# Kernel optimization log

Measured on AMD Instinct MI355X. Metric: run time of the kernel, lower is better.

Reference implementation:

```python
import jax, jax.numpy as jnp
import numpy as np

MAX_SEQ_LEN = 512          # offset added to pairwise diffs
NUM_HEADS = 12             # per-table embedding dim and fused output dim
TABLE_SIZE = 2 * MAX_SEQ_LEN + 1  # 1025
BATCH, SEQ = 4, 512


def setup_inputs() -> dict:
    key = jax.random.key(0)
    ks = jax.random.split(key, 8)
    pos_s = jnp.sort(jax.random.randint(ks[0], (BATCH, SEQ), 0, MAX_SEQ_LEN, dtype=jnp.int32), axis=-1)
    pos_e = jnp.sort(jax.random.randint(ks[1], (BATCH, SEQ), 0, MAX_SEQ_LEN, dtype=jnp.int32), axis=-1)
    pe_ss = jax.random.normal(ks[2], (TABLE_SIZE, NUM_HEADS), dtype=jnp.float32)
    pe_se = jax.random.normal(ks[3], (TABLE_SIZE, NUM_HEADS), dtype=jnp.float32)
    pe_es = jax.random.normal(ks[4], (TABLE_SIZE, NUM_HEADS), dtype=jnp.float32)
    pe_ee = jax.random.normal(ks[5], (TABLE_SIZE, NUM_HEADS), dtype=jnp.float32)
    W = jax.random.normal(ks[6], (4 * NUM_HEADS, NUM_HEADS), dtype=jnp.float32) / np.sqrt(4 * NUM_HEADS)
    b = jax.random.normal(ks[7], (NUM_HEADS,), dtype=jnp.float32) * 0.01
    return {"pos_s": pos_s, "pos_e": pos_e, "pe_ss": pe_ss, "pe_se": pe_se,
            "pe_es": pe_es, "pe_ee": pe_ee, "W": W, "b": b}


def reference(pos_s, pos_e, pe_ss, pe_se, pe_es, pe_ee, W, b):
    # pairwise distance indices, each [B, S, S], values in [0, 2*MAX_SEQ_LEN]
    idx_ss = pos_s[:, :, None] - pos_s[:, None, :] + MAX_SEQ_LEN
    idx_se = pos_s[:, :, None] - pos_e[:, None, :] + MAX_SEQ_LEN
    idx_es = pos_e[:, :, None] - pos_s[:, None, :] + MAX_SEQ_LEN
    idx_ee = pos_e[:, :, None] - pos_e[:, None, :] + MAX_SEQ_LEN
    # four gathers -> [B, S, S, H] each; concat on feature axis -> [B, S, S, 4H]
    pe4 = jnp.concatenate([pe_ss[idx_ss], pe_se[idx_se], pe_es[idx_es], pe_ee[idx_ee]], axis=-1)
    # Linear(4H -> H) + ReLU, then permute to [B, H, S, S]
    fused = jax.nn.relu(jnp.einsum('bijf,fh->bijh', pe4, W) + b)
    return jnp.transpose(fused, (0, 3, 1, 2))
```

## Files before the change

kernel.cpp:

```cpp
#include <hip/hip_runtime.h>

#define MAX_SEQ_LEN 512
#define NUM_HEADS 12
#define TABLE_SIZE 1025
#define BATCH 4
#define SEQ 512

__global__ void proj_tables_kernel(const float* __restrict__ pe_ss,
                                   const float* __restrict__ pe_se,
                                   const float* __restrict__ pe_es,
                                   const float* __restrict__ pe_ee,
                                   const float* __restrict__ W,
                                   const float* __restrict__ bias,
                                   float* __restrict__ proj) {
    int tid = blockIdx.x * blockDim.x + threadIdx.x;
    if (tid >= 4 * TABLE_SIZE) return;
    int t   = tid / TABLE_SIZE;
    int idx = tid - t * TABLE_SIZE;

    const float* pe = (t == 0 ? pe_ss : t == 1 ? pe_se : t == 2 ? pe_es : pe_ee)
                      + idx * NUM_HEADS;
    float pev[NUM_HEADS];
#pragma unroll
    for (int f = 0; f < NUM_HEADS; ++f) pev[f] = pe[f];

    float* out = proj + (size_t)tid * NUM_HEADS;
#pragma unroll
    for (int h = 0; h < NUM_HEADS; ++h) {
        float acc = (t == 0) ? bias[h] : 0.0f;
#pragma unroll
        for (int f = 0; f < NUM_HEADS; ++f)
            acc += pev[f] * W[(t * NUM_HEADS + f) * NUM_HEADS + h];
        out[h] = acc;
    }
}

__global__ __launch_bounds__(128)
void fuse_kernel(const int* __restrict__ pos_s,
                 const int* __restrict__ pos_e,
                 const float* __restrict__ proj,
                 float* __restrict__ out) {
    const int bi = blockIdx.x;
    const int b  = bi >> 9;
    const int i  = bi & (SEQ - 1);

    const int ps_i = pos_s[b * SEQ + i];
    const int pe_i = pos_e[b * SEQ + i];

    const int j0 = threadIdx.x * 4;
    const int4 js4 = *reinterpret_cast<const int4*>(pos_s + b * SEQ + j0);
    const int4 je4 = *reinterpret_cast<const int4*>(pos_e + b * SEQ + j0);
    const int jsa[4] = {js4.x, js4.y, js4.z, js4.w};
    const int jea[4] = {je4.x, je4.y, je4.z, je4.w};

    const float* __restrict__ pss = proj;
    const float* __restrict__ pse = proj + 1 * TABLE_SIZE * NUM_HEADS;
    const float* __restrict__ pes = proj + 2 * TABLE_SIZE * NUM_HEADS;
    const float* __restrict__ pee = proj + 3 * TABLE_SIZE * NUM_HEADS;

    float acc[4][NUM_HEADS];

#pragma unroll
    for (int k = 0; k < 4; ++k) {
        const int iss = ps_i - jsa[k] + MAX_SEQ_LEN;
        const int ise = ps_i - jea[k] + MAX_SEQ_LEN;
        const int ies = pe_i - jsa[k] + MAX_SEQ_LEN;
        const int iee = pe_i - jea[k] + MAX_SEQ_LEN;

        const float4* r0 = reinterpret_cast<const float4*>(pss + iss * NUM_HEADS);
        const float4* r1 = reinterpret_cast<const float4*>(pse + ise * NUM_HEADS);
        const float4* r2 = reinterpret_cast<const float4*>(pes + ies * NUM_HEADS);
        const float4* r3 = reinterpret_cast<const float4*>(pee + iee * NUM_HEADS);

        float4 a0 = r0[0], a1 = r0[1], a2 = r0[2];
        float4 b0 = r1[0], b1 = r1[1], b2 = r1[2];
        float4 c0 = r2[0], c1 = r2[1], c2 = r2[2];
        float4 d0 = r3[0], d1 = r3[1], d2 = r3[2];

        acc[k][0]  = a0.x + b0.x + c0.x + d0.x;
        acc[k][1]  = a0.y + b0.y + c0.y + d0.y;
        acc[k][2]  = a0.z + b0.z + c0.z + d0.z;
        acc[k][3]  = a0.w + b0.w + c0.w + d0.w;
        acc[k][4]  = a1.x + b1.x + c1.x + d1.x;
        acc[k][5]  = a1.y + b1.y + c1.y + d1.y;
        acc[k][6]  = a1.z + b1.z + c1.z + d1.z;
        acc[k][7]  = a1.w + b1.w + c1.w + d1.w;
        acc[k][8]  = a2.x + b2.x + c2.x + d2.x;
        acc[k][9]  = a2.y + b2.y + c2.y + d2.y;
        acc[k][10] = a2.z + b2.z + c2.z + d2.z;
        acc[k][11] = a2.w + b2.w + c2.w + d2.w;
    }

    float* obase = out + (((size_t)b * NUM_HEADS) * SEQ + i) * SEQ + j0;
#pragma unroll
    for (int h = 0; h < NUM_HEADS; ++h) {
        float4 v;
        v.x = fmaxf(acc[0][h], 0.0f);
        v.y = fmaxf(acc[1][h], 0.0f);
        v.z = fmaxf(acc[2][h], 0.0f);
        v.w = fmaxf(acc[3][h], 0.0f);
        *reinterpret_cast<float4*>(obase + (size_t)h * SEQ * SEQ) = v;
    }
}

extern "C" void kernel_launch(void* const* d_in, const int* in_sizes, int n_in,
                              void* d_out, int out_size, void* d_ws, size_t ws_size,
                              hipStream_t stream) {
    const int*   pos_s = (const int*)d_in[0];
    const int*   pos_e = (const int*)d_in[1];
    const float* pe_ss = (const float*)d_in[2];
    const float* pe_se = (const float*)d_in[3];
    const float* pe_es = (const float*)d_in[4];
    const float* pe_ee = (const float*)d_in[5];
    const float* W     = (const float*)d_in[6];
    const float* bias  = (const float*)d_in[7];
    float* out  = (float*)d_out;
    float* proj = (float*)d_ws;

    {
        int total = 4 * TABLE_SIZE;
        int block = 256;
        int grid  = (total + block - 1) / block;
        proj_tables_kernel<<<grid, block, 0, stream>>>(pe_ss, pe_se, pe_es, pe_ee,
                                                       W, bias, proj);
    }

    {
        dim3 grid(BATCH * SEQ);
        dim3 block(128);
        fuse_kernel<<<grid, block, 0, stream>>>(pos_s, pos_e, proj, out);
    }
}
```

Measured before the change: 114.1 us.

## Stage per-row summed projection windows in LDS before pairwise gather

Each block, which handles one (b,i) row, now loads the 512-entry window of projected tables that its fixed pos_s[i] and pos_e[i] can reach. It pre-adds ss+es and se+ee into two LDS arrays, so each output element needs two LDS row reads instead of four scattered global reads. Blocks grow to 256 threads with two j per thread and float2 stores. The exchange is a per-block staging pass of about 48KB of global reads plus a barrier, and narrower output stores.

```diff
diff --git a/kernel.cpp b/kernel.cpp
--- a/kernel.cpp
+++ b/kernel.cpp
@@ -5,6 +5,9 @@
 #define TABLE_SIZE 1025
 #define BATCH 4
 #define SEQ 512
+#define ROWF 12
+#define WIN 512
+#define F4_PER_WIN (WIN * ROWF / 4)
 
 __global__ void proj_tables_kernel(const float* __restrict__ pe_ss,
                                    const float* __restrict__ pe_se,
@@ -24,82 +27,82 @@
 #pragma unroll
     for (int f = 0; f < NUM_HEADS; ++f) pev[f] = pe[f];
 
-    float* out = proj + (size_t)tid * NUM_HEADS;
+    float* outp = proj + (size_t)tid * NUM_HEADS;
 #pragma unroll
     for (int h = 0; h < NUM_HEADS; ++h) {
         float acc = (t == 0) ? bias[h] : 0.0f;
 #pragma unroll
         for (int f = 0; f < NUM_HEADS; ++f)
             acc += pev[f] * W[(t * NUM_HEADS + f) * NUM_HEADS + h];
-        out[h] = acc;
+        outp[h] = acc;
     }
 }
 
-__global__ __launch_bounds__(128)
+__global__ __launch_bounds__(256)
 void fuse_kernel(const int* __restrict__ pos_s,
                  const int* __restrict__ pos_e,
                  const float* __restrict__ proj,
                  float* __restrict__ out) {
+    __shared__ float4 ldsA[F4_PER_WIN];
+    __shared__ float4 ldsB[F4_PER_WIN];
+
     const int bi = blockIdx.x;
     const int b  = bi >> 9;
     const int i  = bi & (SEQ - 1);
 
-    const int ps_i = pos_s[b * SEQ + i];
-    const int pe_i = pos_e[b * SEQ + i];
+    const int ps = pos_s[b * SEQ + i];
+    const int pe = pos_e[b * SEQ + i];
 
-    const int j0 = threadIdx.x * 4;
-    const int4 js4 = *reinterpret_cast<const int4*>(pos_s + b * SEQ + j0);
-    const int4 je4 = *reinterpret_cast<const int4*>(pos_e + b * SEQ + j0);
-    const int jsa[4] = {js4.x, js4.y, js4.z, js4.w};
-    const int jea[4] = {je4.x, je4.y, je4.z, je4.w};
+    const int j0 = threadIdx.x * 2;
+    const int2 js = *reinterpret_cast<const int2*>(pos_s + b * SEQ + j0);
+    const int2 je = *reinterpret_cast<const int2*>(pos_e + b * SEQ + j0);
 
-    const float* __restrict__ pss = proj;
-    const float* __restrict__ pse = proj + 1 * TABLE_SIZE * NUM_HEADS;
-    const float* __restrict__ pes = proj + 2 * TABLE_SIZE * NUM_HEADS;
-    const float* __restrict__ pee = proj + 3 * TABLE_SIZE * NUM_HEADS;
-
-    float acc[4][NUM_HEADS];
+    const float4* __restrict__ wss = reinterpret_cast<const float4*>(
+        proj + ((size_t)0 * TABLE_SIZE + ps + 1) * ROWF);
+    const float4* __restrict__ wse = reinterpret_cast<const float4*>(
+        proj + ((size_t)1 * TABLE_SIZE + ps + 1) * ROWF);
+    const float4* __restrict__ wes = reinterpret_cast<const float4*>(
+        proj + ((size_t)2 * TABLE_SIZE + pe + 1) * ROWF);
+    const float4* __restrict__ wee = reinterpret_cast<const float4*>(
+        proj + ((size_t)3 * TABLE_SIZE + pe + 1) * ROWF);
 
 #pragma unroll
-    for (int k = 0; k < 4; ++k) {
-        const int iss = ps_i - jsa[k] + MAX_SEQ_LEN;
-        const int ise = ps_i - jea[k] + MAX_SEQ_LEN;
-        const int ies = pe_i - jsa[k] + MAX_SEQ_LEN;
-        const int iee = pe_i - jea[k] + MAX_SEQ_LEN;
+    for (int m = threadIdx.x; m < F4_PER_WIN; m += 256) {
+        float4 x = wss[m], y = wes[m];
+        ldsA[m] = make_float4(x.x + y.x, x.y + y.y, x.z + y.z, x.w + y.w);
+        float4 u = wse[m], v = wee[m];
+        ldsB[m] = make_float4(u.x + v.x, u.y + v.y, u.z + v.z, u.w + v.w);
+    }
+    __syncthreads();
 
-        const float4* r0 = reinterpret_cast<const float4*>(pss + iss * NUM_HEADS);
-        const float4* r1 = reinterpret_cast<const float4*>(pse + ise * NUM_HEADS);
-        const float4* r2 = reinterpret_cast<const float4*>(pes + ies * NUM_HEADS);
-        const float4* r3 = reinterpret_cast<const float4*>(pee + iee * NUM_HEADS);
-
-        float4 a0 = r0[0], a1 = r0[1], a2 = r0[2];
-        float4 b0 = r1[0], b1 = r1[1], b2 = r1[2];
-        float4 c0 = r2[0], c1 = r2[1], c2 = r2[2];
-        float4 d0 = r3[0], d1 = r3[1], d2 = r3[2];
-
-        acc[k][0]  = a0.x + b0.x + c0.x + d0.x;
-        acc[k][1]  = a0.y + b0.y + c0.y + d0.y;
-        acc[k][2]  = a0.z + b0.z + c0.z + d0.z;
-        acc[k][3]  = a0.w + b0.w + c0.w + d0.w;
-        acc[k][4]  = a1.x + b1.x + c1.x + d1.x;
-        acc[k][5]  = a1.y + b1.y + c1.y + d1.y;
-        acc[k][6]  = a1.z + b1.z + c1.z + d1.z;
-        acc[k][7]  = a1.w + b1.w + c1.w + d1.w;
-        acc[k][8]  = a2.x + b2.x + c2.x + d2.x;
-        acc[k][9]  = a2.y + b2.y + c2.y + d2.y;
-        acc[k][10] = a2.z + b2.z + c2.z + d2.z;
-        acc[k][11] = a2.w + b2.w + c2.w + d2.w;
+    float r[2][NUM_HEADS];
+#pragma unroll
+    for (int k = 0; k < 2; ++k) {
+        const int rA = (WIN - 1) - (k ? js.y : js.x);
+        const int rB = (WIN - 1) - (k ? je.y : je.x);
+        const float4* a  = ldsA + rA * 3;
+        const float4* bb = ldsB + rB * 3;
+        float4 a0 = a[0], a1 = a[1], a2 = a[2];
+        float4 b0 = bb[0], b1 = bb[1], b2 = bb[2];
+        r[k][0]  = fmaxf(a0.x + b0.x, 0.0f);
+        r[k][1]  = fmaxf(a0.y + b0.y, 0.0f);
+        r[k][2]  = fmaxf(a0.z + b0.z, 0.0f);
+        r[k][3]  = fmaxf(a0.w + b0.w, 0.0f);
+        r[k][4]  = fmaxf(a1.x + b1.x, 0.0f);
+        r[k][5]  = fmaxf(a1.y + b1.y, 0.0f);
+        r[k][6]  = fmaxf(a1.z + b1.z, 0.0f);
+        r[k][7]  = fmaxf(a1.w + b1.w, 0.0f);
+        r[k][8]  = fmaxf(a2.x + b2.x, 0.0f);
+        r[k][9]  = fmaxf(a2.y + b2.y, 0.0f);
+        r[k][10] = fmaxf(a2.z + b2.z, 0.0f);
+        r[k][11] = fmaxf(a2.w + b2.w, 0.0f);
     }
 
     float* obase = out + (((size_t)b * NUM_HEADS) * SEQ + i) * SEQ + j0;
 #pragma unroll
     for (int h = 0; h < NUM_HEADS; ++h) {
-        float4 v;
-        v.x = fmaxf(acc[0][h], 0.0f);
-        v.y = fmaxf(acc[1][h], 0.0f);
-        v.z = fmaxf(acc[2][h], 0.0f);
-        v.w = fmaxf(acc[3][h], 0.0f);
-        *reinterpret_cast<float4*>(obase + (size_t)h * SEQ * SEQ) = v;
+        *reinterpret_cast<float2*>(obase + (size_t)h * SEQ * SEQ) =
+            make_float2(r[0][h], r[1][h]);
     }
 }
 
@@ -124,10 +127,9 @@
         proj_tables_kernel<<<grid, block, 0, stream>>>(pe_ss, pe_se, pe_es, pe_ee,
                                                        W, bias, proj);
     }
-
     {
         dim3 grid(BATCH * SEQ);
-        dim3 block(128);
+        dim3 block(256);
         fuse_kernel<<<grid, block, 0, stream>>>(pos_s, pos_e, proj, out);
     }
 }
```

Result: faster. 97.15 us (-14.9%).
